# Performance work log

Hardware: AMD Instinct MI355X
Metric: run time of the kernel (lower is better)

Reference implementation:

```python
import jax, jax.numpy as jnp
import numpy as np
from jax import lax

GRAVITY = 9.8
DT = 0.1
MAX_STEPS = 200


def _conv(x, w, b):
    # x: [N,C,H,W], w: [O,I,3,3] (PyTorch OIHW), padding=1 -> SAME
    y = lax.conv_general_dilated(x, w, window_strides=(1, 1), padding='SAME',
                                 dimension_numbers=('NCHW', 'OIHW', 'NCHW'))
    return y + b[None, :, None, None]


def _maxpool2(x):
    return lax.reduce_window(x, -jnp.inf, lax.max,
                             window_dimensions=(1, 1, 2, 2),
                             window_strides=(1, 1, 2, 2), padding='VALID')


def setup_inputs() -> dict:
    key = jax.random.key(0)
    ks = jax.random.split(key, 12)
    B = 256
    x = jax.random.normal(ks[0], (B, 12, 128, 128), dtype=jnp.float32)

    def he(k, shape, fan_in):
        return jax.random.normal(k, shape, dtype=jnp.float32) * np.float32(np.sqrt(2.0 / fan_in))

    w1 = he(ks[1], (32, 12, 3, 3), 12 * 9); b1 = jnp.zeros((32,), jnp.float32)
    w2 = he(ks[2], (64, 32, 3, 3), 32 * 9); b2 = jnp.zeros((64,), jnp.float32)
    w3 = he(ks[3], (64, 64, 3, 3), 64 * 9); b3 = jnp.zeros((64,), jnp.float32)
    w4 = he(ks[4], (64, 64, 3, 3), 64 * 9); b4 = jnp.zeros((64,), jnp.float32)
    wl1 = he(ks[5], (128, 64 * 8 * 8), 64 * 8 * 8); bl1 = jnp.zeros((128,), jnp.float32)
    wl2 = he(ks[6], (4, 128), 128); bl2 = jnp.zeros((4,), jnp.float32)
    return {'x': x, 'w1': w1, 'b1': b1, 'w2': w2, 'b2': b2, 'w3': w3, 'b3': b3,
            'w4': w4, 'b4': b4, 'wl1': wl1, 'bl1': bl1, 'wl2': wl2, 'bl2': bl2}


def _forward(x, w1, b1, w2, b2, w3, b3, w4, b4, wl1, bl1, wl2, bl2):
    h = _maxpool2(jax.nn.relu(_conv(x, w1, b1)))   # [B,32,64,64]
    h = _maxpool2(jax.nn.relu(_conv(h, w2, b2)))   # [B,64,32,32]
    h = _maxpool2(jax.nn.relu(_conv(h, w3, b3)))   # [B,64,16,16]
    h = _maxpool2(jax.nn.relu(_conv(h, w4, b4)))   # [B,64,8,8]
    h = h.reshape(h.shape[0], -1)                  # [B,4096]
    h = jax.nn.relu(h @ wl1.T + bl1)               # [B,128]
    state = h @ wl2.T + bl2                        # [B,4]

    px, py, vx, vy = state[:, 0], state[:, 1], state[:, 2], state[:, 3]

    def step(carry, _):
        cx, cy, cvy = carry
        nvy = cvy - GRAVITY * DT
        nx = cx + vx * DT
        ny = jnp.maximum(cy + nvy * DT, 0.0)
        return (nx, ny, nvy), None

    (fx, _, _), _ = lax.scan(step, (px, py, vy), None, length=MAX_STEPS)
    return fx


def reference(x, w1, b1, w2, b2, w3, b3, w4, b4, wl1, bl1, wl2, bl2):
    return _forward(x, w1, b1, w2, b2, w3, b3, w4, b4, wl1, bl1, wl2, bl2)
```

## Files before the change

kernel.cpp:

```cpp
#include <hip/hip_runtime.h>


typedef _Float16 f16;
typedef _Float16 f16x8 __attribute__((ext_vector_type(8)));
typedef _Float16 f16x4 __attribute__((ext_vector_type(4)));
typedef float f32x4 __attribute__((ext_vector_type(4)));
typedef float f32x16 __attribute__((ext_vector_type(16)));

__global__ __launch_bounds__(512)
void pack_weights(const float* __restrict__ w1, const float* __restrict__ w2,
                  const float* __restrict__ w3, const float* __restrict__ w4,
                  f16* __restrict__ apack) {
  int idx = blockIdx.x * 512 + threadIdx.x;
  int frag = idx >> 9;
  int e = idx & 511;
  int lane = e >> 3, j = e & 7;
  float v = 0.f;
  if (frag < 9) {
    int kh = frag / 3, kw = frag % 3;
    int oc = lane & 31;
    int ic = (lane >> 5) * 8 + j;
    if (ic < 12) v = w1[((oc * 12 + ic) * 3 + kh) * 3 + kw];
  } else if (frag < 45) {
    int f = frag - 9;
    int sh = f >> 2, og = f & 3;
    int kh = sh / 3, kw = sh % 3;
    int row16 = lane & 15, kg = lane >> 4;
    int oc = og * 16 + row16;
    int ic = kg * 8 + j;
    v = w2[((oc * 32 + ic) * 3 + kh) * 3 + kw];
  } else {
    const float* w = (frag < 117) ? w3 : w4;
    int f = frag - ((frag < 117) ? 45 : 117);
    int sk = f >> 2, og = f & 3;
    int sh = sk >> 1, ks = sk & 1;
    int kh = sh / 3, kw = sh % 3;
    int row16 = lane & 15, kg = lane >> 4;
    int oc = og * 16 + row16;
    int ic = ks * 32 + kg * 8 + j;
    v = w[((oc * 64 + ic) * 3 + kh) * 3 + kw];
  }
  apack[idx] = (f16)v;
}

__global__ __launch_bounds__(512)
void conv1_mfma(const float* __restrict__ x, const f16* __restrict__ apack,
                const float* __restrict__ bias, f16* __restrict__ hout) {
  constexpr int W = 128, H = 128;
  constexpr int PADB = 48, ROWB = 130 * PADB;
  constexpr int TPB = 8;
  __shared__ char smem[6 * ROWB];
  const int tid = threadIdx.x;
  const int n = blockIdx.y;
  const int R0 = blockIdx.x * (TPB * 4);

  if (tid < 36) {
    int slot = tid / 6, r = tid % 6;
    int px = (r >= 3) ? 129 : 0;
    int ch = r % 3;
    *(float4*)(smem + slot * ROWB + px * PADB + ch * 16) =
        make_float4(0.f, 0.f, 0.f, 0.f);
  }

  const int g = tid >> 4;
  const int l16 = tid & 15;
  const int Q = l16 >> 2, q = l16 & 3;

  auto load_row = [&](int ri) -> float4 {
    float4 v = make_float4(0.f, 0.f, 0.f, 0.f);
    if (l16 < 12 && ri >= 0 && ri < H)
      v = *(const float4*)(x + ((size_t)(n * 12 + l16) * H + ri) * W + g * 4);
    return v;
  };
  auto xpose_write = [&](float4 av, int slot) {
    float4 t1, t2;
    {
      float sx = __shfl_xor(av.x, 1), sy = __shfl_xor(av.y, 1);
      float sz = __shfl_xor(av.z, 1), sw = __shfl_xor(av.w, 1);
      bool odd = q & 1;
      t1.x = odd ? sy : av.x;  t1.y = odd ? av.y : sx;
      t1.z = odd ? sw : av.z;  t1.w = odd ? av.w : sz;
    }
    {
      float sx = __shfl_xor(t1.x, 2), sy = __shfl_xor(t1.y, 2);
      float sz = __shfl_xor(t1.z, 2), sw = __shfl_xor(t1.w, 2);
      bool hi2 = q & 2;
      t2.x = hi2 ? sz : t1.x;  t2.y = hi2 ? sw : t1.y;
      t2.z = hi2 ? t1.z : sx;  t2.w = hi2 ? t1.w : sy;
    }
    f16x4 h = { (f16)t2.x, (f16)t2.y, (f16)t2.z, (f16)t2.w };
    *(f16x4*)(smem + slot * ROWB + (g * 4 + q + 1) * PADB + Q * 8) = h;
  };

  const int wv = tid >> 6, l = tid & 63;
  const int rp = wv >> 2;
  const int pxb = (wv & 3) * 32;
  const int rl0 = rp * 2;
  const int ln = l & 31;
  const int hi = l >> 5;

  f16x8 A[9];
#pragma unroll
  for (int ks = 0; ks < 9; ++ks)
    A[ks] = *(const f16x8*)(apack + ((ks << 9) + (l << 3)));

  float4 a[6];
#pragma unroll
  for (int i = 0; i < 6; ++i) a[i] = load_row(R0 - 1 + i);
#pragma unroll
  for (int i = 0; i < 6; ++i) xpose_write(a[i], i);
  __syncthreads();

  int s0 = 0;
  for (int t = 0; t < TPB; ++t) {
    if (t + 1 < TPB) {
#pragma unroll
      for (int i = 0; i < 4; ++i) a[i] = load_row(R0 + 4 * t + 5 + i);
    }
    f32x16 acc0 = (f32x16)0.f, acc1 = (f32x16)0.f;
#pragma unroll
    for (int kw = 0; kw < 3; ++kw) {
      const char* bcol = smem + (pxb + ln + kw) * PADB + hi * 16;
      f16x8 R[4];
#pragma unroll
      for (int j = 0; j < 4; ++j) {
        int sl = s0 + rl0 + j; if (sl >= 6) sl -= 6; if (sl >= 6) sl -= 6;
        R[j] = *(const f16x8*)(bcol + sl * ROWB);
      }
#pragma unroll
      for (int kh = 0; kh < 3; ++kh) {
        acc0 = __builtin_amdgcn_mfma_f32_32x32x16_f16(A[kh * 3 + kw], R[kh],     acc0, 0, 0, 0);
        acc1 = __builtin_amdgcn_mfma_f32_32x32x16_f16(A[kh * 3 + kw], R[kh + 1], acc1, 0, 0, 0);
      }
    }
    {
      const int pr = (R0 >> 1) + 2 * t + rp;
#pragma unroll
      for (int gg = 0; gg < 4; ++gg) {
        float v[4];
#pragma unroll
        for (int c = 0; c < 4; ++c) {
          float m = fmaxf(acc0[gg * 4 + c], acc1[gg * 4 + c]);
          v[c] = fmaxf(m, __shfl_xor(m, 1));
        }
        if ((l & 1) == 0) {
          const int pw = (pxb + ln) >> 1;
          const int oc0 = gg * 8 + hi * 4;
          f16x4 pk;
#pragma unroll
          for (int c = 0; c < 4; ++c)
            pk[c] = (f16)fmaxf(v[c] + bias[oc0 + c], 0.f);
          *(f16x4*)(hout + (((size_t)(n * 64 + pr) * 64 + pw) * 32 + oc0)) = pk;
        }
      }
    }
    __syncthreads();
    if (t + 1 < TPB) {
#pragma unroll
      for (int i = 0; i < 4; ++i) {
        int sl = s0 + i; if (sl >= 6) sl -= 6;
        xpose_write(a[i], sl);
      }
      __syncthreads();
    }
    s0 += 4; if (s0 >= 6) s0 -= 6;
  }
}

template<int C, int W, int H, int BR, int KS, int PADB, int PGn, bool NCHW_OUT>
__global__ __launch_bounds__(256)
void conv_shift(const f16* __restrict__ hin, const f16* __restrict__ apack,
                const float* __restrict__ bias, void* __restrict__ hout) {
  constexpr int SR = BR + 2;
  constexpr int ROWB = (W + 2) * PADB;
  __shared__ char smem[SR * ROWB];
  const int tid = threadIdx.x;
  const int n = blockIdx.y;
  const int r0 = blockIdx.x * BR;
  constexpr int CPC = C / 8;
  constexpr int TOTC = SR * (W + 2) * CPC;
  constexpr int NITER = (TOTC + 255) / 256;
  {
    float4 stg[NITER];
#pragma unroll
    for (int it = 0; it < NITER; ++it) {
      const int t = tid + it * 256;
      float4 v = make_float4(0.f, 0.f, 0.f, 0.f);
      if (t < TOTC) {
        int sr = t / ((W + 2) * CPC);
        int rem = t - sr * ((W + 2) * CPC);
        int px = rem / CPC;
        int kc = rem - px * CPC;
        int ri = r0 + sr - 1;
        int gx = px - 1;
        if (ri >= 0 && ri < H && gx >= 0 && gx < W)
          v = *(const float4*)(hin + (((size_t)(n * H + ri) * W + gx) * C + kc * 8));
      }
      stg[it] = v;
    }
#pragma unroll
    for (int it = 0; it < NITER; ++it) {
      const int t = tid + it * 256;
      if (t < TOTC) {
        int sr = t / ((W + 2) * CPC);
        int rem = t - sr * ((W + 2) * CPC);
        int px = rem / CPC;
        int kc = rem - px * CPC;
        *(float4*)(smem + sr * ROWB + px * PADB + kc * 16) = stg[it];
      }
    }
  }
  __syncthreads();

  const int wv = tid >> 6, l = tid & 63;
  constexpr int WPP = W / (16 * PGn);
  const int rp = wv / WPP;
  const int pxb = (wv % WPP) * 16 * PGn;
  const int rl0 = rp * 2;
  const int lp = l & 15, kg = l >> 4;
  const int px0 = pxb + lp;

  f32x4 acc[2][PGn][4];
#pragma unroll
  for (int a = 0; a < 2; ++a)
#pragma unroll
    for (int b = 0; b < PGn; ++b)
#pragma unroll
      for (int c = 0; c < 4; ++c)
        acc[a][b][c] = (f32x4){0.f, 0.f, 0.f, 0.f};

#pragma unroll
  for (int sh = 0; sh < 9; ++sh) {
    const int kh = sh / 3, kw = sh % 3;
    f16x8 A[KS][4];
#pragma unroll
    for (int ks = 0; ks < KS; ++ks)
#pragma unroll
      for (int og = 0; og < 4; ++og)
        A[ks][og] = *(const f16x8*)(apack + ((((sh * KS + ks) * 4 + og) << 9) + (l << 3)));
#pragma unroll
    for (int rowi = 0; rowi < 2; ++rowi) {
      const char* base = smem + (rl0 + rowi + kh) * ROWB;
#pragma unroll
      for (int pg = 0; pg < PGn; ++pg) {
#pragma unroll
        for (int ks = 0; ks < KS; ++ks) {
          f16x8 B = *(const f16x8*)(base + (px0 + pg * 16 + kw) * PADB + ks * 64 + kg * 16);
#pragma unroll
          for (int og = 0; og < 4; ++og)
            acc[rowi][pg][og] =
                __builtin_amdgcn_mfma_f32_16x16x32_f16(A[ks][og], B, acc[rowi][pg][og], 0, 0, 0);
        }
      }
    }
  }
  constexpr int PH = H / 2, PW = W / 2;
  const int pr = blockIdx.x * (BR / 2) + rp;
#pragma unroll
  for (int pg = 0; pg < PGn; ++pg) {
#pragma unroll
    for (int og = 0; og < 4; ++og) {
      float v[4];
#pragma unroll
      for (int c = 0; c < 4; ++c) {
        float m = fmaxf(acc[0][pg][og][c], acc[1][pg][og][c]);
        v[c] = fmaxf(m, __shfl_xor(m, 1));
      }
      if ((l & 1) == 0) {
        const int pw = (pxb + pg * 16 + lp) >> 1;
        const int oc0 = og * 16 + kg * 4;
        if constexpr (NCHW_OUT) {
          float* o = (float*)hout;
#pragma unroll
          for (int c = 0; c < 4; ++c)
            o[(((size_t)n * 64 + oc0 + c) * PH + pr) * PW + pw] =
                fmaxf(v[c] + bias[oc0 + c], 0.f);
        } else {
          f16x4 pk;
#pragma unroll
          for (int c = 0; c < 4; ++c)
            pk[c] = (f16)fmaxf(v[c] + bias[oc0 + c], 0.f);
          *(f16x4*)((f16*)hout + (((size_t)(n * PH + pr) * PW + pw) * 64 + oc0)) = pk;
        }
      }
    }
  }
}

__global__ __launch_bounds__(1024)
void fc_head(const float* __restrict__ h4, const float* __restrict__ wl1,
             const float* __restrict__ bl1, const float* __restrict__ wl2,
             const float* __restrict__ bl2, float* __restrict__ out) {
  __shared__ float rows[2][4096];
  __shared__ float red[8 * 128 * 2];
  __shared__ float red2[2 * 128];
  const int tid = threadIdx.x;
  const int b0 = blockIdx.x * 2;
  {
    const float4* src = (const float4*)(h4 + (size_t)b0 * 4096);
    float4* dst = (float4*)rows;
    for (int t = tid; t < 2048; t += 1024) dst[t] = src[t];
  }
  __syncthreads();

  const int nn = tid & 127;
  const int ks = tid >> 7;
  const float4* wp = (const float4*)(wl1 + (size_t)nn * 4096 + ks * 512);
  const float4* x0 = (const float4*)(&rows[0][ks * 512]);
  const float4* x1 = (const float4*)(&rows[1][ks * 512]);
  float s0 = 0.f, s1 = 0.f;
#pragma unroll 8
  for (int i = 0; i < 128; ++i) {
    float4 w = wp[i], a = x0[i], b = x1[i];
    s0 = fmaf(w.x, a.x, fmaf(w.y, a.y, fmaf(w.z, a.z, fmaf(w.w, a.w, s0))));
    s1 = fmaf(w.x, b.x, fmaf(w.y, b.y, fmaf(w.z, b.z, fmaf(w.w, b.w, s1))));
  }
  red[(ks * 128 + nn) * 2 + 0] = s0;
  red[(ks * 128 + nn) * 2 + 1] = s1;
  __syncthreads();

  if (tid < 256) {
    const int r = tid >> 7, n2 = tid & 127;
    float h = bl1[n2];
#pragma unroll
    for (int k = 0; k < 8; ++k) h += red[(k * 128 + n2) * 2 + r];
    h = fmaxf(h, 0.f);
    red2[r * 128 + n2] = h * (wl2[n2] + 20.0f * wl2[256 + n2]);
  }
  __syncthreads();
#pragma unroll
  for (int s = 64; s > 0; s >>= 1) {
    if (tid < 2 * s) {
      int r = tid / s, i = tid - r * s;
      red2[r * 128 + i] += red2[r * 128 + i + s];
    }
    __syncthreads();
  }
  if (tid < 2) out[b0 + tid] = red2[tid * 128] + bl2[0] + 20.0f * bl2[2];
}

extern "C" void kernel_launch(void* const* d_in, const int* in_sizes, int n_in,
                              void* d_out, int out_size, void* d_ws, size_t ws_size,
                              hipStream_t stream) {
  const float* x   = (const float*)d_in[0];
  const float* w1  = (const float*)d_in[1];
  const float* b1  = (const float*)d_in[2];
  const float* w2  = (const float*)d_in[3];
  const float* b2  = (const float*)d_in[4];
  const float* w3  = (const float*)d_in[5];
  const float* b3  = (const float*)d_in[6];
  const float* w4  = (const float*)d_in[7];
  const float* b4  = (const float*)d_in[8];
  const float* wl1 = (const float*)d_in[9];
  const float* bl1 = (const float*)d_in[10];
  const float* wl2 = (const float*)d_in[11];
  const float* bl2 = (const float*)d_in[12];
  float* out = (float*)d_out;
  char* ws = (char*)d_ws;

  f16* apack = (f16*)ws;
  f16* h1 = (f16*)(ws + (1u << 20));
  f16* h2 = (f16*)(ws + 68157440u);
  f16* h3 = (f16*)(ws + 101711872u);
  float* h4 = (float*)(ws + 110100480u);

  pack_weights<<<189, 512, 0, stream>>>(w1, w2, w3, w4, apack);
  conv1_mfma<<<dim3(4, 256), 512, 0, stream>>>(x, apack, b1, h1);
  conv_shift<32, 64, 64, 4, 1, 80, 2, false><<<dim3(16, 256), 256, 0, stream>>>(
      h1, apack + 9 * 512, b2, (void*)h2);
  conv_shift<64, 32, 32, 8, 2, 144, 2, false><<<dim3(4, 256), 256, 0, stream>>>(
      h2, apack + 45 * 512, b3, (void*)h3);
  conv_shift<64, 16, 16, 8, 2, 144, 1, true><<<dim3(2, 256), 256, 0, stream>>>(
      h3, apack + 117 * 512, b4, (void*)h4);
  fc_head<<<128, 1024, 0, stream>>>(h4, wl1, bl1, wl2, bl2, out);
}
```

Measured before the change: 228.7 us.

## Use 32x32x16 MFMA tiles for conv2 and conv3 with repacked weights

Adds a conv_shift32 kernel in which each wave covers 32 pixels by 64 output channels using 32x32x16 MFMA instead of the 16-row tiles of the old conv_shift. Weights for conv2 and conv3 are repacked into the matching 32-row fragment layout. Each B fragment read from LDS now feeds two MFMAs, one per output-channel group, which is meant to cut LDS traffic and instruction count. In exchange it uses more accumulator registers, which may lower occupancy. A redundant wraparound check in conv1 is also dropped.

```diff
diff --git a/kernel.cpp b/kernel.cpp
--- a/kernel.cpp
+++ b/kernel.cpp
@@ -23,22 +23,31 @@
     if (ic < 12) v = w1[((oc * 12 + ic) * 3 + kh) * 3 + kw];
   } else if (frag < 45) {
     int f = frag - 9;
-    int sh = f >> 2, og = f & 3;
+    int ocg = f & 1;
+    int sk = f >> 1;
+    int ks = sk & 1, sh = sk >> 1;
     int kh = sh / 3, kw = sh % 3;
-    int row16 = lane & 15, kg = lane >> 4;
-    int oc = og * 16 + row16;
-    int ic = kg * 8 + j;
+    int oc = ocg * 32 + (lane & 31);
+    int ic = ks * 16 + (lane >> 5) * 8 + j;
     v = w2[((oc * 32 + ic) * 3 + kh) * 3 + kw];
+  } else if (frag < 117) {
+    int f = frag - 45;
+    int ocg = f & 1;
+    int sk = f >> 1;
+    int ks = sk & 3, sh = sk >> 2;
+    int kh = sh / 3, kw = sh % 3;
+    int oc = ocg * 32 + (lane & 31);
+    int ic = ks * 16 + (lane >> 5) * 8 + j;
+    v = w3[((oc * 64 + ic) * 3 + kh) * 3 + kw];
   } else {
-    const float* w = (frag < 117) ? w3 : w4;
-    int f = frag - ((frag < 117) ? 45 : 117);
+    int f = frag - 117;
     int sk = f >> 2, og = f & 3;
     int sh = sk >> 1, ks = sk & 1;
     int kh = sh / 3, kw = sh % 3;
     int row16 = lane & 15, kg = lane >> 4;
     int oc = og * 16 + row16;
     int ic = ks * 32 + kg * 8 + j;
-    v = w[((oc * 64 + ic) * 3 + kh) * 3 + kw];
+    v = w4[((oc * 64 + ic) * 3 + kh) * 3 + kw];
   }
   apack[idx] = (f16)v;
 }
@@ -124,7 +133,7 @@
       f16x8 R[4];
 #pragma unroll
       for (int j = 0; j < 4; ++j) {
-        int sl = s0 + rl0 + j; if (sl >= 6) sl -= 6; if (sl >= 6) sl -= 6;
+        int sl = s0 + rl0 + j; if (sl >= 6) sl -= 6;
         R[j] = *(const f16x8*)(bcol + sl * ROWB);
       }
 #pragma unroll
@@ -164,6 +173,110 @@
       __syncthreads();
     }
     s0 += 4; if (s0 >= 6) s0 -= 6;
+  }
+}
+
+template<int C, int W, int H, int BR, int PADB>
+__global__ __launch_bounds__(256)
+void conv_shift32(const f16* __restrict__ hin, const f16* __restrict__ apack,
+                  const float* __restrict__ bias, f16* __restrict__ hout) {
+  constexpr int KS16 = C / 16;
+  constexpr int SR = BR + 2;
+  constexpr int ROWB = (W + 2) * PADB;
+  __shared__ char smem[SR * ROWB];
+  const int tid = threadIdx.x;
+  const int n = blockIdx.y;
+  const int r0 = blockIdx.x * BR;
+  constexpr int CPC = C / 8;
+  constexpr int TOTC = SR * (W + 2) * CPC;
+  constexpr int NITER = (TOTC + 255) / 256;
+  {
+    float4 stg[NITER];
+#pragma unroll
+    for (int it = 0; it < NITER; ++it) {
+      const int t = tid + it * 256;
+      float4 v = make_float4(0.f, 0.f, 0.f, 0.f);
+      if (t < TOTC) {
+        int sr = t / ((W + 2) * CPC);
+        int rem = t - sr * ((W + 2) * CPC);
+        int px = rem / CPC;
+        int kc = rem - px * CPC;
+        int ri = r0 + sr - 1;
+        int gx = px - 1;
+        if (ri >= 0 && ri < H && gx >= 0 && gx < W)
+          v = *(const float4*)(hin + (((size_t)(n * H + ri) * W + gx) * C + kc * 8));
+      }
+      stg[it] = v;
+    }
+#pragma unroll
+    for (int it = 0; it < NITER; ++it) {
+      const int t = tid + it * 256;
+      if (t < TOTC) {
+        int sr = t / ((W + 2) * CPC);
+        int rem = t - sr * ((W + 2) * CPC);
+        int px = rem / CPC;
+        int kc = rem - px * CPC;
+        *(float4*)(smem + sr * ROWB + px * PADB + kc * 16) = stg[it];
+      }
+    }
+  }
+  __syncthreads();
+
+  const int wv = tid >> 6, l = tid & 63;
+  constexpr int WPP = W / 32;
+  const int rp = wv / WPP;
+  const int pxb = (wv % WPP) * 32;
+  const int rl0 = rp * 2;
+  const int ln = l & 31;
+  const int hi = l >> 5;
+  const int px0 = pxb + ln;
+
+  f32x16 acc[2][2];
+  acc[0][0] = (f32x16)0.f; acc[0][1] = (f32x16)0.f;
+  acc[1][0] = (f32x16)0.f; acc[1][1] = (f32x16)0.f;
+
+#pragma unroll
+  for (int sh = 0; sh < 9; ++sh) {
+    const int kh = sh / 3, kw = sh % 3;
+    f16x8 A[KS16][2];
+#pragma unroll
+    for (int ks = 0; ks < KS16; ++ks)
+#pragma unroll
+      for (int ocg = 0; ocg < 2; ++ocg)
+        A[ks][ocg] = *(const f16x8*)(apack + ((((sh * KS16 + ks) * 2 + ocg) << 9) + (l << 3)));
+#pragma unroll
+    for (int rowi = 0; rowi < 2; ++rowi) {
+      const char* base = smem + (rl0 + rowi + kh) * ROWB + (px0 + kw) * PADB + hi * 16;
+#pragma unroll
+      for (int ks = 0; ks < KS16; ++ks) {
+        f16x8 B = *(const f16x8*)(base + ks * 32);
+        acc[rowi][0] = __builtin_amdgcn_mfma_f32_32x32x16_f16(A[ks][0], B, acc[rowi][0], 0, 0, 0);
+        acc[rowi][1] = __builtin_amdgcn_mfma_f32_32x32x16_f16(A[ks][1], B, acc[rowi][1], 0, 0, 0);
+      }
+    }
+  }
+  constexpr int PH = H / 2, PW = W / 2;
+  const int pr = blockIdx.x * (BR / 2) + rp;
+#pragma unroll
+  for (int ocg = 0; ocg < 2; ++ocg) {
+#pragma unroll
+    for (int gg = 0; gg < 4; ++gg) {
+      float v[4];
+#pragma unroll
+      for (int c = 0; c < 4; ++c) {
+        float m = fmaxf(acc[0][ocg][gg * 4 + c], acc[1][ocg][gg * 4 + c]);
+        v[c] = fmaxf(m, __shfl_xor(m, 1));
+      }
+      if ((l & 1) == 0) {
+        const int pw = (pxb + ln) >> 1;
+        const int oc0 = ocg * 32 + gg * 8 + hi * 4;
+        f16x4 pk;
+#pragma unroll
+        for (int c = 0; c < 4; ++c)
+          pk[c] = (f16)fmaxf(v[c] + bias[oc0 + c], 0.f);
+        *(f16x4*)(hout + (((size_t)(n * PH + pr) * PW + pw) * 64 + oc0)) = pk;
+      }
+    }
   }
 }
 
@@ -366,10 +479,10 @@
 
   pack_weights<<<189, 512, 0, stream>>>(w1, w2, w3, w4, apack);
   conv1_mfma<<<dim3(4, 256), 512, 0, stream>>>(x, apack, b1, h1);
-  conv_shift<32, 64, 64, 4, 1, 80, 2, false><<<dim3(16, 256), 256, 0, stream>>>(
-      h1, apack + 9 * 512, b2, (void*)h2);
-  conv_shift<64, 32, 32, 8, 2, 144, 2, false><<<dim3(4, 256), 256, 0, stream>>>(
-      h2, apack + 45 * 512, b3, (void*)h3);
+  conv_shift32<32, 64, 64, 4, 80><<<dim3(16, 256), 256, 0, stream>>>(
+      h1, apack + 9 * 512, b2, h2);
+  conv_shift32<64, 32, 32, 8, 144><<<dim3(4, 256), 256, 0, stream>>>(
+      h2, apack + 45 * 512, b3, h3);
   conv_shift<64, 16, 16, 8, 2, 144, 1, true><<<dim3(2, 256), 256, 0, stream>>>(
       h3, apack + 117 * 512, b4, (void*)h4);
   fc_head<<<128, 1024, 0, stream>>>(h4, wl1, bl1, wl2, bl2, out);
```

Result: no change. 232.6 us (+1.7%).
